# Optimization experiments

Measured on AMD Instinct MI355X. Metric: run time of the kernel, lower is better.

The kernel has to match this reference:

```python
import jax, jax.numpy as jnp
from jax import lax
import numpy as np

DN = ('NCHW', 'OIHW', 'NCHW')
B, C, H, W = 4, 64, 128, 128


def _conv3x3(x, w, b):
    y = lax.conv_general_dilated(x, w, (1, 1), 'SAME', dimension_numbers=DN)
    return y + b[None, :, None, None]


def _bilinear_gather(x, ys, xs):
    # x: [B,C,H,W]; ys, xs: [B,K,H,W] float sample coordinates (clamped at border)
    b, c, h, w = x.shape
    y0 = jnp.floor(ys)
    x0 = jnp.floor(xs)
    ty = (ys - y0)[:, None]  # [B,1,K,H,W]
    tx = (xs - x0)[:, None]
    y0i = jnp.clip(y0.astype(jnp.int32), 0, h - 1)
    y1i = jnp.clip(y0i + 1, 0, h - 1)
    x0i = jnp.clip(x0.astype(jnp.int32), 0, w - 1)
    x1i = jnp.clip(x0i + 1, 0, w - 1)
    xf = x.reshape(b, c, h * w)

    def g(yi, xi):
        idx = (yi * w + xi).reshape(b, 1, -1)
        v = jnp.take_along_axis(xf, jnp.broadcast_to(idx, (b, c, idx.shape[-1])), axis=2)
        return v.reshape(b, c, *yi.shape[1:])  # [B,C,K,H,W]

    v00 = g(y0i, x0i)
    v01 = g(y0i, x1i)
    v10 = g(y1i, x0i)
    v11 = g(y1i, x1i)
    return v00 * (1 - ty) * (1 - tx) + v01 * (1 - ty) * tx + v10 * ty * (1 - tx) + v11 * ty * tx


def _arconv(x, w_off, b_off, Wk, bk, hw_lo, hw_hi):
    # Adaptive rectangular conv: predict per-pixel (h,w) of the receptive field,
    # bilinearly sample a 3x3 grid scaled by (h/2, w/2), then apply learned 3x3 weights.
    b, c, h, w = x.shape
    hw = jax.nn.sigmoid(_conv3x3(x, w_off, b_off))  # [B,2,H,W]
    rf_h = hw_lo + (hw_hi - hw_lo) * hw[:, 0]       # [B,H,W]
    rf_w = hw_lo + (hw_hi - hw_lo) * hw[:, 1]
    d = jnp.array([-1.0, 0.0, 1.0], x.dtype)
    dyk = jnp.repeat(d, 3)  # [9]
    dxk = jnp.tile(d, 3)    # [9]
    ys = jnp.arange(h, dtype=x.dtype)[None, None, :, None] + dyk[None, :, None, None] * (rf_h[:, None] / 2)
    xs = jnp.arange(w, dtype=x.dtype)[None, None, None, :] + dxk[None, :, None, None] * (rf_w[:, None] / 2)
    samp = _bilinear_gather(x, ys, xs)  # [B,C,9,H,W]
    o = Wk.shape[0]
    return jnp.einsum('bckhw,ock->bohw', samp, Wk.reshape(o, c, 9)) + bk[None, :, None, None]


def setup_inputs() -> dict:
    key = jax.random.key(0)
    ks = jax.random.split(key, 9)
    s = 0.05
    return {
        'x': jax.random.normal(ks[0], (B, C, H, W), jnp.float32),
        'w_off1': jax.random.normal(ks[1], (2, C, 3, 3), jnp.float32) * s,
        'b_off1': jnp.zeros((2,), jnp.float32),
        'W1': jax.random.normal(ks[2], (C, C, 3, 3), jnp.float32) * s,
        'b1': jnp.zeros((C,), jnp.float32),
        'w_off2': jax.random.normal(ks[3], (2, C, 3, 3), jnp.float32) * s,
        'b_off2': jnp.zeros((2,), jnp.float32),
        'W2': jax.random.normal(ks[4], (C, C, 3, 3), jnp.float32) * s,
        'b2': jnp.zeros((C,), jnp.float32),
        'epochs': 200,
        'hw_lo': 1,
        'hw_hi': 9,
    }


def reference(x, w_off1, b_off1, W1, b1, w_off2, b_off2, W2, b2, epochs, hw_lo, hw_hi):
    lo = jnp.float32(hw_lo)
    hi = jnp.float32(hw_hi)
    res = _arconv(x, w_off1, b_off1, W1, b1, lo, hi)
    res = jax.nn.relu(res)
    res = _arconv(res, w_off2, b_off2, W2, b2, lo, hi)
    return x + res
```

## Files before the change

### kernel.cpp

```cpp
#include <hip/hip_runtime.h>
#include <math.h>

#define BB 4
#define CC 64
#define OO 64
#define HH 128
#define WWD 128
#define HWP (HH*WWD)

typedef short bf16x8 __attribute__((ext_vector_type(8)));
typedef float f32x4  __attribute__((ext_vector_type(4)));
typedef float f32x2  __attribute__((ext_vector_type(2)));

__device__ __forceinline__ unsigned short bf16_rne(float f) {
    unsigned u = __float_as_uint(f);
    u += 0x7fffu + ((u >> 16) & 1u);
    return (unsigned short)(u >> 16);
}
__device__ __forceinline__ float bf16_tof(unsigned short h) {
    return __uint_as_float((unsigned)h << 16);
}
__device__ __forceinline__ f32x2 ld2(const float* p) {
    f32x2 r; __builtin_memcpy(&r, p, 2 * sizeof(float)); return r;
}

#define BARRIER_NOVM() do { \
    __builtin_amdgcn_sched_barrier(0); \
    asm volatile("s_waitcnt lgkmcnt(0)"); \
    __builtin_amdgcn_s_barrier(); \
    __builtin_amdgcn_sched_barrier(0); \
} while (0)

__global__ __launch_bounds__(256) void wtrans_kernel(
    const float* __restrict__ W1, const float* __restrict__ W2,
    unsigned short* __restrict__ Wh1, unsigned short* __restrict__ Wl1,
    unsigned short* __restrict__ Wh2, unsigned short* __restrict__ Wl2)
{
    int idx = blockIdx.x * 256 + threadIdx.x;
    const int n = OO * CC * 9;
    const float* src;
    unsigned short *dh, *dl;
    if (idx >= n) { src = W2; dh = Wh2; dl = Wl2; idx -= n; }
    else          { src = W1; dh = Wh1; dl = Wl1; }
    int c = idx & 63;
    int o = (idx >> 6) & 63;
    int k = idx >> 12;
    float w = src[(o * CC + c) * 9 + k];
    unsigned short hi = bf16_rne(w);
    unsigned short lo = bf16_rne(w - bf16_tof(hi));
    dh[idx] = hi;
    dl[idx] = lo;
}

template<int DY, int DX>
__device__ __forceinline__ void issue_tap(
    const float* __restrict__ xbase, int y, int xx0i, float fy, float fx,
    float rh, float rw,
    float (&v00)[16], float (&v01)[16], float (&v10)[16], float (&v11)[16],
    float& w00, float& w01, float& w10, float& w11, bool& xhi)
{
    if (DY == 0 && DX == 0) {
        const float* c00 = xbase + y * WWD + xx0i;
#pragma unroll
        for (int i = 0; i < 16; ++i) v00[i] = c00[i * HWP];
    } else if (DY == 0) {
        float xs = fx + (float)DX * rw;
        float x0f = floorf(xs);
        float tx = xs - x0f;
        int ix0 = min(max((int)x0f, 0), WWD - 1);
        int ix0c = min(ix0, WWD - 2);
        xhi = (ix0 == WWD - 1);
        w00 = 1.f - tx; w01 = tx;
        const float* c00 = xbase + y * WWD + ix0c;
#pragma unroll
        for (int i = 0; i < 16; ++i) {
            f32x2 p = ld2(c00 + i * HWP);
            v00[i] = p.x; v01[i] = p.y;
        }
    } else if (DX == 0) {
        float ys = fy + (float)DY * rh;
        float y0f = floorf(ys);
        float ty = ys - y0f;
        int iy0 = min(max((int)y0f, 0), HH - 1);
        int iy1 = min(iy0 + 1, HH - 1);
        w00 = 1.f - ty; w10 = ty;
        const float* c00 = xbase + iy0 * WWD + xx0i;
        const float* c10 = xbase + iy1 * WWD + xx0i;
#pragma unroll
        for (int i = 0; i < 16; ++i) { v00[i] = c00[i*HWP]; v10[i] = c10[i*HWP]; }
    } else {
        float ys = fy + (float)DY * rh;
        float xs = fx + (float)DX * rw;
        float y0f = floorf(ys), x0f = floorf(xs);
        float ty = ys - y0f, tx = xs - x0f;
        int iy0 = min(max((int)y0f, 0), HH - 1);
        int iy1 = min(iy0 + 1, HH - 1);
        int ix0 = min(max((int)x0f, 0), WWD - 1);
        int ix0c = min(ix0, WWD - 2);
        xhi = (ix0 == WWD - 1);
        w00 = (1.f - ty) * (1.f - tx);
        w01 = (1.f - ty) * tx;
        w10 = ty * (1.f - tx);
        w11 = ty * tx;
        const float* c0 = xbase + iy0 * WWD + ix0c;
        const float* c1 = xbase + iy1 * WWD + ix0c;
#pragma unroll
        for (int i = 0; i < 16; ++i) {
            f32x2 pt = ld2(c0 + i * HWP);
            f32x2 pb = ld2(c1 + i * HWP);
            v00[i] = pt.x; v01[i] = pt.y;
            v10[i] = pb.x; v11[i] = pb.y;
        }
    }
}

template<int DY, int DX>
__device__ __forceinline__ void finish_tap(
    const float (&v00)[16], const float (&v01)[16],
    const float (&v10)[16], const float (&v11)[16],
    float w00, float w01, float w10, float w11, bool xhi,
    unsigned short* sh_dst, unsigned short* sl_dst)
{
    union { unsigned short h[16]; uint4 q[2]; } svh, svl;
#pragma unroll
    for (int i = 0; i < 16; ++i) {
        float s;
        if (DY == 0 && DX == 0) {
            s = v00[i];
        } else if (DY == 0) {
            float a0 = xhi ? v01[i] : v00[i];
            s = w00 * a0 + w01 * v01[i];
        } else if (DX == 0) {
            s = w00 * v00[i] + w10 * v10[i];
        } else {
            float t0 = xhi ? v01[i] : v00[i];
            float b0 = xhi ? v11[i] : v10[i];
            s = w00 * t0 + w01 * v01[i] + w10 * b0 + w11 * v11[i];
        }
        unsigned short hs = bf16_rne(s);
        svh.h[i] = hs;
        svl.h[i] = bf16_rne(s - bf16_tof(hs));
    }
    *(uint4*)sh_dst       = svh.q[0];
    *(uint4*)(sh_dst + 8) = svh.q[1];
    *(uint4*)sl_dst       = svl.q[0];
    *(uint4*)(sl_dst + 8) = svl.q[1];
}

__global__ __launch_bounds__(256) void arconv_kernel(
    const float*          __restrict__ xin,
    const unsigned short* __restrict__ Whi,
    const unsigned short* __restrict__ Wlo,
    const float*          __restrict__ bias,
    const float*          __restrict__ woff,
    const float*          __restrict__ boff,
    const int* __restrict__ lo_p, const int* __restrict__ hi_p,
    const float* __restrict__ resid,
    float* __restrict__ out, int mode)
{
    __shared__ unsigned short sWh[OO * 72];
    __shared__ unsigned short sWl[OO * 72];
    __shared__ unsigned short sSh[64 * 72];
    __shared__ unsigned short sSl[64 * 72];
    __shared__ float srf[2][64];

    int t    = threadIdx.x;
    int bid  = blockIdx.x;
    int blk  = ((bid & 7) << 7) | (bid >> 3);
    int b    = blk >> 8;
    int tile = blk & 255;
    int p0   = tile * 64;
    int y    = p0 >> 7;
    int xb   = p0 & 127;

    int lane = t & 63;
    int wv   = t >> 6;
    int pl   = lane;
    int cq   = wv;
    int nidx = lane & 15;
    int quad = lane >> 4;
    int xx0i = xb + pl;
    float fy = (float)y;
    float fx = (float)xx0i;

    int cqoff = __builtin_amdgcn_readfirstlane(cq * 16 * HWP);
    const float* xbase = xin + (size_t)b * CC * HWP + cqoff;

    {
        float* swA = (float*)sWh;
        float* red = (float*)sSh;
        for (int i = t; i < 2 * CC * 9; i += 256) swA[i] = woff[i];
        __syncthreads();
        float a0 = 0.f, a1 = 0.f;
        {
            const float* xc = xbase;
#pragma unroll 4
            for (int ci = 0; ci < 16; ++ci) {
                int c = cq * 16 + ci;
                const float* w0 = swA + c * 9;
                const float* w1 = swA + (CC + c) * 9;
#pragma unroll
                for (int ky = 0; ky < 3; ++ky) {
                    int yy = y + ky - 1;
                    bool yok = (yy >= 0) && (yy < HH);
#pragma unroll
                    for (int kx = 0; kx < 3; ++kx) {
                        int xx = xx0i + kx - 1;
                        float v = 0.f;
                        if (yok && xx >= 0 && xx < WWD) v = xc[yy * WWD + xx];
                        a0 = fmaf(v, w0[ky * 3 + kx], a0);
                        a1 = fmaf(v, w1[ky * 3 + kx], a1);
                    }
                }
                xc += HWP;
            }
        }
        red[cq * 64 + pl]       = a0;
        red[256 + cq * 64 + pl] = a1;
        __syncthreads();
        if (t < 64) {
            float flo = (float)lo_p[0];
            float fhi = (float)hi_p[0];
            float s0 = red[t] + red[64 + t] + red[128 + t] + red[192 + t] + boff[0];
            float s1 = red[256 + t] + red[320 + t] + red[384 + t] + red[448 + t] + boff[1];
            float g0 = 1.f / (1.f + expf(-s0));
            float g1 = 1.f / (1.f + expf(-s1));
            srf[0][t] = (flo + (fhi - flo) * g0) * 0.5f;
            srf[1][t] = (flo + (fhi - flo) * g1) * 0.5f;
        }
        __syncthreads();
    }
    float rh = srf[0][pl];
    float rw = srf[1][pl];

    f32x4 acc[4] = {};
    float v00[16], v01[16], v10[16], v11[16];
    float w00 = 0.f, w01 = 0.f, w10 = 0.f, w11 = 0.f;
    bool xhi = false;
    uint4 wh0, wh1, wl0, wl1;
    const unsigned short* wgh = Whi;
    const unsigned short* wgl = Wlo;

    unsigned short* shp = &sSh[pl * 72 + cq * 16];
    unsigned short* slp = &sSl[pl * 72 + cq * 16];

#define ISSUE_W() do { \
        const uint4* whs_ = (const uint4*)wgh; \
        const uint4* wls_ = (const uint4*)wgl; \
        wh0 = whs_[t * 2]; wh1 = whs_[t * 2 + 1]; \
        wl0 = wls_[t * 2]; wl1 = wls_[t * 2 + 1]; \
        wgh += OO * CC; wgl += OO * CC; \
    } while (0)

#define WRITE_W() do { \
        unsigned short* dh_ = &sWh[(t >> 2) * 72 + (t & 3) * 16]; \
        unsigned short* dl_ = &sWl[(t >> 2) * 72 + (t & 3) * 16]; \
        *(uint4*)dh_       = wh0; *(uint4*)(dh_ + 8) = wh1; \
        *(uint4*)dl_       = wl0; *(uint4*)(dl_ + 8) = wl1; \
    } while (0)

#define MFMA_TAP() do { \
        _Pragma("unroll") \
        for (int ks = 0; ks < 2; ++ks) { \
            int boff_ = (wv * 16 + nidx) * 72 + quad * 8 + ks * 32; \
            bf16x8 bh = *(const bf16x8*)&sSh[boff_]; \
            bf16x8 bl = *(const bf16x8*)&sSl[boff_]; \
            _Pragma("unroll") \
            for (int mt = 0; mt < 4; ++mt) { \
                int aoff_ = (mt * 16 + nidx) * 72 + quad * 8 + ks * 32; \
                bf16x8 ah = *(const bf16x8*)&sWh[aoff_]; \
                bf16x8 al = *(const bf16x8*)&sWl[aoff_]; \
                acc[mt] = __builtin_amdgcn_mfma_f32_16x16x32_bf16(ah, bh, acc[mt], 0, 0, 0); \
                acc[mt] = __builtin_amdgcn_mfma_f32_16x16x32_bf16(al, bh, acc[mt], 0, 0, 0); \
                acc[mt] = __builtin_amdgcn_mfma_f32_16x16x32_bf16(ah, bl, acc[mt], 0, 0, 0); \
            } \
        } \
    } while (0)

#define STEP(NDY, NDX) do { \
        ISSUE_W(); \
        issue_tap<NDY, NDX>(xbase, y, xx0i, fy, fx, rh, rw, \
                            v00, v01, v10, v11, w00, w01, w10, w11, xhi); \
        MFMA_TAP(); \
        BARRIER_NOVM(); \
        finish_tap<NDY, NDX>(v00, v01, v10, v11, w00, w01, w10, w11, xhi, shp, slp); \
        WRITE_W(); \
        BARRIER_NOVM(); \
    } while (0)

    ISSUE_W();
    issue_tap<-1, -1>(xbase, y, xx0i, fy, fx, rh, rw,
                      v00, v01, v10, v11, w00, w01, w10, w11, xhi);
    finish_tap<-1, -1>(v00, v01, v10, v11, w00, w01, w10, w11, xhi, shp, slp);
    WRITE_W();
    __syncthreads();

    STEP(-1,  0);
    STEP(-1,  1);
    STEP( 0, -1);
    STEP( 0,  0);
    STEP( 0,  1);
    STEP( 1, -1);
    STEP( 1,  0);
    STEP( 1,  1);
    MFMA_TAP();

#undef STEP
#undef MFMA_TAP
#undef WRITE_W
#undef ISSUE_W

    int px = wv * 16 + nidx;
#pragma unroll
    for (int mt = 0; mt < 4; ++mt) {
#pragma unroll
        for (int r = 0; r < 4; ++r) {
            int o = mt * 16 + quad * 4 + r;
            float v = acc[mt][r] + bias[o];
            size_t idx = (size_t)(b * OO + o) * HWP + p0 + px;
            if (mode == 1) v = fmaxf(v, 0.f);
            else           v += resid[idx];
            out[idx] = v;
        }
    }
}

extern "C" void kernel_launch(void* const* d_in, const int* in_sizes, int n_in,
                              void* d_out, int out_size, void* d_ws, size_t ws_size,
                              hipStream_t stream) {
    const float* x      = (const float*)d_in[0];
    const float* w_off1 = (const float*)d_in[1];
    const float* b_off1 = (const float*)d_in[2];
    const float* W1     = (const float*)d_in[3];
    const float* b1     = (const float*)d_in[4];
    const float* w_off2 = (const float*)d_in[5];
    const float* b_off2 = (const float*)d_in[6];
    const float* W2     = (const float*)d_in[7];
    const float* b2     = (const float*)d_in[8];
    const int*   lo_p   = (const int*)d_in[10];
    const int*   hi_p   = (const int*)d_in[11];
    float* outp = (float*)d_out;

    float* wsf = (float*)d_ws;
    float* t1  = wsf;
    unsigned short* Wh1 = (unsigned short*)(t1 + (size_t)BB * CC * HWP);
    unsigned short* Wl1 = Wh1 + OO * CC * 9;
    unsigned short* Wh2 = Wl1 + OO * CC * 9;
    unsigned short* Wl2 = Wh2 + OO * CC * 9;

    wtrans_kernel<<<288, 256, 0, stream>>>(W1, W2, Wh1, Wl1, Wh2, Wl2);

    arconv_kernel<<<1024, 256, 0, stream>>>(x, Wh1, Wl1, b1, w_off1, b_off1,
                                            lo_p, hi_p, nullptr, t1, 1);

    arconv_kernel<<<1024, 256, 0, stream>>>(t1, Wh2, Wl2, b2, w_off2, b_off2,
                                            lo_p, hi_p, x, outp, 2);
}
```

Before: 246.0 us.

## Remove LDS staging: gather samples directly into MFMA fragments, weights from global

Each lane now builds its own MFMA B-fragment directly in registers from bilinear gathers. Weight A-fragments are read straight from global memory (L1/L2 cached) instead of being staged through shared memory with barriers. The offset conv reduction uses cross-lane shuffles instead of an LDS reduction, and a software pipeline splits channels into halves so one half's gather overlaps the other's MFMAs. All shared memory and __syncthreads are removed and launch bounds request 4 blocks per CU. The trade-off is more global and cache traffic for weights and higher register pressure.

```diff
diff --git a/kernel.cpp b/kernel.cpp
--- a/kernel.cpp
+++ b/kernel.cpp
@@ -23,13 +23,9 @@
 __device__ __forceinline__ f32x2 ld2(const float* p) {
     f32x2 r; __builtin_memcpy(&r, p, 2 * sizeof(float)); return r;
 }
-
-#define BARRIER_NOVM() do { \
-    __builtin_amdgcn_sched_barrier(0); \
-    asm volatile("s_waitcnt lgkmcnt(0)"); \
-    __builtin_amdgcn_s_barrier(); \
-    __builtin_amdgcn_sched_barrier(0); \
-} while (0)
+__device__ __forceinline__ bf16x8 ldw16(const unsigned short* p) {
+    bf16x8 r; __builtin_memcpy(&r, p, 16); return r;
+}
 
 __global__ __launch_bounds__(256) void wtrans_kernel(
     const float* __restrict__ W1, const float* __restrict__ W2,
@@ -52,42 +48,37 @@
     dl[idx] = lo;
 }
 
+struct TapC {
+    float w00, w01, w10, w11;
+    int off0, off1;
+    int xhi;
+};
+
 template<int DY, int DX>
-__device__ __forceinline__ void issue_tap(
-    const float* __restrict__ xbase, int y, int xx0i, float fy, float fx,
-    float rh, float rw,
-    float (&v00)[16], float (&v01)[16], float (&v10)[16], float (&v11)[16],
-    float& w00, float& w01, float& w10, float& w11, bool& xhi)
-{
+__device__ __forceinline__ TapC mk_coords(int y, int xg, float fy, float fx,
+                                          float rh, float rw)
+{
+    TapC C; C.w00 = C.w01 = C.w10 = C.w11 = 0.f; C.off0 = C.off1 = 0; C.xhi = 0;
     if (DY == 0 && DX == 0) {
-        const float* c00 = xbase + y * WWD + xx0i;
-#pragma unroll
-        for (int i = 0; i < 16; ++i) v00[i] = c00[i * HWP];
+        C.off0 = y * WWD + xg;
     } else if (DY == 0) {
         float xs = fx + (float)DX * rw;
         float x0f = floorf(xs);
         float tx = xs - x0f;
         int ix0 = min(max((int)x0f, 0), WWD - 1);
         int ix0c = min(ix0, WWD - 2);
-        xhi = (ix0 == WWD - 1);
-        w00 = 1.f - tx; w01 = tx;
-        const float* c00 = xbase + y * WWD + ix0c;
-#pragma unroll
-        for (int i = 0; i < 16; ++i) {
-            f32x2 p = ld2(c00 + i * HWP);
-            v00[i] = p.x; v01[i] = p.y;
-        }
+        C.xhi = (ix0 == WWD - 1);
+        C.w00 = 1.f - tx; C.w01 = tx;
+        C.off0 = y * WWD + ix0c;
     } else if (DX == 0) {
         float ys = fy + (float)DY * rh;
         float y0f = floorf(ys);
         float ty = ys - y0f;
         int iy0 = min(max((int)y0f, 0), HH - 1);
         int iy1 = min(iy0 + 1, HH - 1);
-        w00 = 1.f - ty; w10 = ty;
-        const float* c00 = xbase + iy0 * WWD + xx0i;
-        const float* c10 = xbase + iy1 * WWD + xx0i;
-#pragma unroll
-        for (int i = 0; i < 16; ++i) { v00[i] = c00[i*HWP]; v10[i] = c10[i*HWP]; }
+        C.w00 = 1.f - ty; C.w10 = ty;
+        C.off0 = iy0 * WWD + xg;
+        C.off1 = iy1 * WWD + xg;
     } else {
         float ys = fy + (float)DY * rh;
         float xs = fx + (float)DX * rw;
@@ -97,57 +88,79 @@
         int iy1 = min(iy0 + 1, HH - 1);
         int ix0 = min(max((int)x0f, 0), WWD - 1);
         int ix0c = min(ix0, WWD - 2);
-        xhi = (ix0 == WWD - 1);
-        w00 = (1.f - ty) * (1.f - tx);
-        w01 = (1.f - ty) * tx;
-        w10 = ty * (1.f - tx);
-        w11 = ty * tx;
-        const float* c0 = xbase + iy0 * WWD + ix0c;
-        const float* c1 = xbase + iy1 * WWD + ix0c;
-#pragma unroll
-        for (int i = 0; i < 16; ++i) {
-            f32x2 pt = ld2(c0 + i * HWP);
-            f32x2 pb = ld2(c1 + i * HWP);
-            v00[i] = pt.x; v01[i] = pt.y;
-            v10[i] = pb.x; v11[i] = pb.y;
-        }
-    }
+        C.xhi = (ix0 == WWD - 1);
+        C.w00 = (1.f - ty) * (1.f - tx);
+        C.w01 = (1.f - ty) * tx;
+        C.w10 = ty * (1.f - tx);
+        C.w11 = ty * tx;
+        C.off0 = iy0 * WWD + ix0c;
+        C.off1 = iy1 * WWD + ix0c;
+    }
+    return C;
 }
 
 template<int DY, int DX>
-__device__ __forceinline__ void finish_tap(
-    const float (&v00)[16], const float (&v01)[16],
-    const float (&v10)[16], const float (&v11)[16],
-    float w00, float w01, float w10, float w11, bool xhi,
-    unsigned short* sh_dst, unsigned short* sl_dst)
-{
-    union { unsigned short h[16]; uint4 q[2]; } svh, svl;
-#pragma unroll
-    for (int i = 0; i < 16; ++i) {
+__device__ __forceinline__ void gather_half(
+    const float* __restrict__ xq, const TapC& C,
+    float (&g0)[8], float (&g1)[8], float (&g2)[8], float (&g3)[8])
+{
+    if (DY == 0 && DX == 0) {
+#pragma unroll
+        for (int i = 0; i < 8; ++i) g0[i] = xq[C.off0 + i * HWP];
+    } else if (DY == 0) {
+#pragma unroll
+        for (int i = 0; i < 8; ++i) {
+            f32x2 p = ld2(xq + C.off0 + i * HWP);
+            g0[i] = p.x; g1[i] = p.y;
+        }
+    } else if (DX == 0) {
+#pragma unroll
+        for (int i = 0; i < 8; ++i) {
+            g0[i] = xq[C.off0 + i * HWP];
+            g2[i] = xq[C.off1 + i * HWP];
+        }
+    } else {
+#pragma unroll
+        for (int i = 0; i < 8; ++i) {
+            f32x2 pt = ld2(xq + C.off0 + i * HWP);
+            f32x2 pb = ld2(xq + C.off1 + i * HWP);
+            g0[i] = pt.x; g1[i] = pt.y;
+            g2[i] = pb.x; g3[i] = pb.y;
+        }
+    }
+}
+
+template<int DY, int DX>
+__device__ __forceinline__ void combine_half(
+    const TapC& C,
+    const float (&g0)[8], const float (&g1)[8],
+    const float (&g2)[8], const float (&g3)[8],
+    bf16x8& bh, bf16x8& bl)
+{
+    union { unsigned short h[8]; bf16x8 v; } uh, ul;
+#pragma unroll
+    for (int i = 0; i < 8; ++i) {
         float s;
         if (DY == 0 && DX == 0) {
-            s = v00[i];
+            s = g0[i];
         } else if (DY == 0) {
-            float a0 = xhi ? v01[i] : v00[i];
-            s = w00 * a0 + w01 * v01[i];
+            float a0 = C.xhi ? g1[i] : g0[i];
+            s = C.w00 * a0 + C.w01 * g1[i];
         } else if (DX == 0) {
-            s = w00 * v00[i] + w10 * v10[i];
+            s = C.w00 * g0[i] + C.w10 * g2[i];
         } else {
-            float t0 = xhi ? v01[i] : v00[i];
-            float b0 = xhi ? v11[i] : v10[i];
-            s = w00 * t0 + w01 * v01[i] + w10 * b0 + w11 * v11[i];
+            float t0 = C.xhi ? g1[i] : g0[i];
+            float b0 = C.xhi ? g3[i] : g2[i];
+            s = C.w00 * t0 + C.w01 * g1[i] + C.w10 * b0 + C.w11 * g3[i];
         }
         unsigned short hs = bf16_rne(s);
-        svh.h[i] = hs;
-        svl.h[i] = bf16_rne(s - bf16_tof(hs));
-    }
-    *(uint4*)sh_dst       = svh.q[0];
-    *(uint4*)(sh_dst + 8) = svh.q[1];
-    *(uint4*)sl_dst       = svl.q[0];
-    *(uint4*)(sl_dst + 8) = svl.q[1];
-}
-
-__global__ __launch_bounds__(256) void arconv_kernel(
+        uh.h[i] = hs;
+        ul.h[i] = bf16_rne(s - bf16_tof(hs));
+    }
+    bh = uh.v; bl = ul.v;
+}
+
+__global__ __launch_bounds__(256, 4) void arconv_kernel(
     const float*          __restrict__ xin,
     const unsigned short* __restrict__ Whi,
     const unsigned short* __restrict__ Wlo,
@@ -158,12 +171,6 @@
     const float* __restrict__ resid,
     float* __restrict__ out, int mode)
 {
-    __shared__ unsigned short sWh[OO * 72];
-    __shared__ unsigned short sWl[OO * 72];
-    __shared__ unsigned short sSh[64 * 72];
-    __shared__ unsigned short sSl[64 * 72];
-    __shared__ float srf[2][64];
-
     int t    = threadIdx.x;
     int bid  = blockIdx.x;
     int blk  = ((bid & 7) << 7) | (bid >> 3);
@@ -175,154 +182,123 @@
 
     int lane = t & 63;
     int wv   = t >> 6;
-    int pl   = lane;
-    int cq   = wv;
     int nidx = lane & 15;
     int quad = lane >> 4;
-    int xx0i = xb + pl;
+    int xg   = xb + wv * 16 + nidx;
     float fy = (float)y;
-    float fx = (float)xx0i;
-
-    int cqoff = __builtin_amdgcn_readfirstlane(cq * 16 * HWP);
-    const float* xbase = xin + (size_t)b * CC * HWP + cqoff;
-
+    float fx = (float)xg;
+
+    const float* xbase = xin + (size_t)b * CC * HWP;
+
+    float a0 = 0.f, a1 = 0.f;
     {
-        float* swA = (float*)sWh;
-        float* red = (float*)sSh;
-        for (int i = t; i < 2 * CC * 9; i += 256) swA[i] = woff[i];
-        __syncthreads();
-        float a0 = 0.f, a1 = 0.f;
-        {
-            const float* xc = xbase;
 #pragma unroll 4
-            for (int ci = 0; ci < 16; ++ci) {
-                int c = cq * 16 + ci;
-                const float* w0 = swA + c * 9;
-                const float* w1 = swA + (CC + c) * 9;
-#pragma unroll
-                for (int ky = 0; ky < 3; ++ky) {
-                    int yy = y + ky - 1;
-                    bool yok = (yy >= 0) && (yy < HH);
-#pragma unroll
-                    for (int kx = 0; kx < 3; ++kx) {
-                        int xx = xx0i + kx - 1;
-                        float v = 0.f;
-                        if (yok && xx >= 0 && xx < WWD) v = xc[yy * WWD + xx];
-                        a0 = fmaf(v, w0[ky * 3 + kx], a0);
-                        a1 = fmaf(v, w1[ky * 3 + kx], a1);
-                    }
+        for (int ci = 0; ci < 16; ++ci) {
+            int c = quad * 16 + ci;
+            const float* xc = xbase + (size_t)c * HWP;
+            const float* w0 = woff + c * 9;
+            const float* w1 = woff + (CC + c) * 9;
+#pragma unroll
+            for (int ky = 0; ky < 3; ++ky) {
+                int yy = y + ky - 1;
+                bool yok = (yy >= 0) && (yy < HH);
+#pragma unroll
+                for (int kx = 0; kx < 3; ++kx) {
+                    int xx = xg + kx - 1;
+                    float v = 0.f;
+                    if (yok && xx >= 0 && xx < WWD) v = xc[yy * WWD + xx];
+                    a0 = fmaf(v, w0[ky * 3 + kx], a0);
+                    a1 = fmaf(v, w1[ky * 3 + kx], a1);
                 }
-                xc += HWP;
             }
         }
-        red[cq * 64 + pl]       = a0;
-        red[256 + cq * 64 + pl] = a1;
-        __syncthreads();
-        if (t < 64) {
-            float flo = (float)lo_p[0];
-            float fhi = (float)hi_p[0];
-            float s0 = red[t] + red[64 + t] + red[128 + t] + red[192 + t] + boff[0];
-            float s1 = red[256 + t] + red[320 + t] + red[384 + t] + red[448 + t] + boff[1];
-            float g0 = 1.f / (1.f + expf(-s0));
-            float g1 = 1.f / (1.f + expf(-s1));
-            srf[0][t] = (flo + (fhi - flo) * g0) * 0.5f;
-            srf[1][t] = (flo + (fhi - flo) * g1) * 0.5f;
-        }
-        __syncthreads();
-    }
-    float rh = srf[0][pl];
-    float rw = srf[1][pl];
-
-    f32x4 acc[4] = {};
-    float v00[16], v01[16], v10[16], v11[16];
-    float w00 = 0.f, w01 = 0.f, w10 = 0.f, w11 = 0.f;
-    bool xhi = false;
-    uint4 wh0, wh1, wl0, wl1;
-    const unsigned short* wgh = Whi;
-    const unsigned short* wgl = Wlo;
-
-    unsigned short* shp = &sSh[pl * 72 + cq * 16];
-    unsigned short* slp = &sSl[pl * 72 + cq * 16];
-
-#define ISSUE_W() do { \
-        const uint4* whs_ = (const uint4*)wgh; \
-        const uint4* wls_ = (const uint4*)wgl; \
-        wh0 = whs_[t * 2]; wh1 = whs_[t * 2 + 1]; \
-        wl0 = wls_[t * 2]; wl1 = wls_[t * 2 + 1]; \
-        wgh += OO * CC; wgl += OO * CC; \
+        a0 += __shfl_xor(a0, 16); a0 += __shfl_xor(a0, 32);
+        a1 += __shfl_xor(a1, 16); a1 += __shfl_xor(a1, 32);
+    }
+    float flo = (float)lo_p[0];
+    float fhi = (float)hi_p[0];
+    float rh = (flo + (fhi - flo) / (1.f + expf(-(a0 + boff[0])))) * 0.5f;
+    float rw = (flo + (fhi - flo) / (1.f + expf(-(a1 + boff[1])))) * 0.5f;
+
+    const float* xq0 = xbase + (size_t)(quad * 8) * HWP;
+    const float* xq1 = xq0 + (size_t)32 * HWP;
+    const int fragbase = nidx * CC + quad * 8;
+
+    f32x4 acc0 = {}, acc1 = {}, acc2 = {}, acc3 = {};
+    float gA0[8], gA1[8], gA2[8], gA3[8];
+    float gB0[8], gB1[8], gB2[8], gB3[8];
+    TapC C;
+
+#define MFMA(a, bfr, c) __builtin_amdgcn_mfma_f32_16x16x32_bf16(a, bfr, c, 0, 0, 0)
+#define MFMA_BLOCK(WH, WL, bh, bl) do { \
+        bf16x8 ah0 = ldw16(WH),        al0 = ldw16(WL); \
+        bf16x8 ah1 = ldw16(WH + 1024), al1 = ldw16(WL + 1024); \
+        bf16x8 ah2 = ldw16(WH + 2048), al2 = ldw16(WL + 2048); \
+        bf16x8 ah3 = ldw16(WH + 3072), al3 = ldw16(WL + 3072); \
+        acc0 = MFMA(ah0, bh, acc0); acc0 = MFMA(al0, bh, acc0); acc0 = MFMA(ah0, bl, acc0); \
+        acc1 = MFMA(ah1, bh, acc1); acc1 = MFMA(al1, bh, acc1); acc1 = MFMA(ah1, bl, acc1); \
+        acc2 = MFMA(ah2, bh, acc2); acc2 = MFMA(al2, bh, acc2); acc2 = MFMA(ah2, bl, acc2); \
+        acc3 = MFMA(ah3, bh, acc3); acc3 = MFMA(al3, bh, acc3); acc3 = MFMA(ah3, bl, acc3); \
     } while (0)
 
-#define WRITE_W() do { \
-        unsigned short* dh_ = &sWh[(t >> 2) * 72 + (t & 3) * 16]; \
-        unsigned short* dl_ = &sWl[(t >> 2) * 72 + (t & 3) * 16]; \
-        *(uint4*)dh_       = wh0; *(uint4*)(dh_ + 8) = wh1; \
-        *(uint4*)dl_       = wl0; *(uint4*)(dl_ + 8) = wl1; \
-    } while (0)
-
-#define MFMA_TAP() do { \
+#define TAP(K, DYc, DXc, NDY, NDX, ISLAST) \
+    { \
+         \
+        gather_half<DYc, DXc>(xq1, C, gB0, gB1, gB2, gB3); \
+        { \
+            bf16x8 bh, bl; \
+            combine_half<DYc, DXc>(C, gA0, gA1, gA2, gA3, bh, bl); \
+            const unsigned short* whk = Whi + (K) * OO * CC + fragbase; \
+            const unsigned short* wlk = Wlo + (K) * OO * CC + fragbase; \
+            MFMA_BLOCK(whk, wlk, bh, bl); \
+        } \
+         \
+        { \
+            TapC Cn = C; \
+            if (!(ISLAST)) { \
+                Cn = mk_coords<NDY, NDX>(y, xg, fy, fx, rh, rw); \
+                gather_half<NDY, NDX>(xq0, Cn, gA0, gA1, gA2, gA3); \
+            } \
+            bf16x8 bh, bl; \
+            combine_half<DYc, DXc>(C, gB0, gB1, gB2, gB3, bh, bl); \
+            const unsigned short* whk = Whi + (K) * OO * CC + fragbase + 32; \
+            const unsigned short* wlk = Wlo + (K) * OO * CC + fragbase + 32; \
+            MFMA_BLOCK(whk, wlk, bh, bl); \
+            C = Cn; \
+        } \
+    }
+
+    C = mk_coords<-1, -1>(y, xg, fy, fx, rh, rw);
+    gather_half<-1, -1>(xq0, C, gA0, gA1, gA2, gA3);
+
+    TAP(0, -1, -1, -1,  0, 0)
+    TAP(1, -1,  0, -1,  1, 0)
+    TAP(2, -1,  1,  0, -1, 0)
+    TAP(3,  0, -1,  0,  0, 0)
+    TAP(4,  0,  0,  0,  1, 0)
+    TAP(5,  0,  1,  1, -1, 0)
+    TAP(6,  1, -1,  1,  0, 0)
+    TAP(7,  1,  0,  1,  1, 0)
+    TAP(8,  1,  1,  0,  0, 1)
+
+#undef TAP
+#undef MFMA_BLOCK
+#undef MFMA
+
+    int px = p0 + wv * 16 + nidx;
+#define EPI(MT, ACCV) do { \
         _Pragma("unroll") \
-        for (int ks = 0; ks < 2; ++ks) { \
-            int boff_ = (wv * 16 + nidx) * 72 + quad * 8 + ks * 32; \
-            bf16x8 bh = *(const bf16x8*)&sSh[boff_]; \
-            bf16x8 bl = *(const bf16x8*)&sSl[boff_]; \
-            _Pragma("unroll") \
-            for (int mt = 0; mt < 4; ++mt) { \
-                int aoff_ = (mt * 16 + nidx) * 72 + quad * 8 + ks * 32; \
-                bf16x8 ah = *(const bf16x8*)&sWh[aoff_]; \
-                bf16x8 al = *(const bf16x8*)&sWl[aoff_]; \
-                acc[mt] = __builtin_amdgcn_mfma_f32_16x16x32_bf16(ah, bh, acc[mt], 0, 0, 0); \
-                acc[mt] = __builtin_amdgcn_mfma_f32_16x16x32_bf16(al, bh, acc[mt], 0, 0, 0); \
-                acc[mt] = __builtin_amdgcn_mfma_f32_16x16x32_bf16(ah, bl, acc[mt], 0, 0, 0); \
-            } \
+        for (int r = 0; r < 4; ++r) { \
+            int o = (MT) * 16 + quad * 4 + r; \
+            float v = ACCV[r] + bias[o]; \
+            size_t idx = (size_t)(b * OO + o) * HWP + px; \
+            if (mode == 1) v = fmaxf(v, 0.f); \
+            else           v += resid[idx]; \
+            out[idx] = v; \
         } \
     } while (0)
-
-#define STEP(NDY, NDX) do { \
-        ISSUE_W(); \
-        issue_tap<NDY, NDX>(xbase, y, xx0i, fy, fx, rh, rw, \
-                            v00, v01, v10, v11, w00, w01, w10, w11, xhi); \
-        MFMA_TAP(); \
-        BARRIER_NOVM(); \
-        finish_tap<NDY, NDX>(v00, v01, v10, v11, w00, w01, w10, w11, xhi, shp, slp); \
-        WRITE_W(); \
-        BARRIER_NOVM(); \
-    } while (0)
-
-    ISSUE_W();
-    issue_tap<-1, -1>(xbase, y, xx0i, fy, fx, rh, rw,
-                      v00, v01, v10, v11, w00, w01, w10, w11, xhi);
-    finish_tap<-1, -1>(v00, v01, v10, v11, w00, w01, w10, w11, xhi, shp, slp);
-    WRITE_W();
-    __syncthreads();
-
-    STEP(-1,  0);
-    STEP(-1,  1);
-    STEP( 0, -1);
-    STEP( 0,  0);
-    STEP( 0,  1);
-    STEP( 1, -1);
-    STEP( 1,  0);
-    STEP( 1,  1);
-    MFMA_TAP();
-
-#undef STEP
-#undef MFMA_TAP
-#undef WRITE_W
-#undef ISSUE_W
-
-    int px = wv * 16 + nidx;
-#pragma unroll
-    for (int mt = 0; mt < 4; ++mt) {
-#pragma unroll
-        for (int r = 0; r < 4; ++r) {
-            int o = mt * 16 + quad * 4 + r;
-            float v = acc[mt][r] + bias[o];
-            size_t idx = (size_t)(b * OO + o) * HWP + p0 + px;
-            if (mode == 1) v = fmaxf(v, 0.f);
-            else           v += resid[idx];
-            out[idx] = v;
-        }
-    }
+    EPI(0, acc0); EPI(1, acc1); EPI(2, acc2); EPI(3, acc3);
+#undef EPI
 }
 
 extern "C" void kernel_launch(void* const* d_in, const int* in_sizes, int n_in,
```

New measurement: 420.7 us. +71.0%, slower.
